# Optimization experiments

Measured on AMD Instinct MI355X. Metric: run time of the kernel, lower is better.

## Reference

```python
import jax, jax.numpy as jnp
import numpy as np

B, S, D, H, MLP = 8, 1024, 768, 12, 3072
HD = D // H
EPS = 1e-5


def setup_inputs() -> dict:
    key = jax.random.key(0)
    ks = jax.random.split(key, 5)
    sd = lambda fan_in: 1.0 / np.sqrt(fan_in)
    return {
        "x": jax.random.normal(ks[0], (B, S, D), jnp.float32),
        "w_qkv": jax.random.normal(ks[1], (D, 3 * D), jnp.float32) * sd(D),
        "w_out": jax.random.normal(ks[2], (D, D), jnp.float32) * sd(D),
        "b_out": jnp.zeros((D,), jnp.float32),
        "w1": jax.random.normal(ks[3], (D, MLP), jnp.float32) * sd(D),
        "b1": jnp.zeros((MLP,), jnp.float32),
        "w2": jax.random.normal(ks[4], (MLP, D), jnp.float32) * sd(MLP),
        "b2": jnp.zeros((D,), jnp.float32),
    }


def _instance_norm(x):
    # torch InstanceNorm2d on a 3D [B,S,D] tensor treats it as unbatched (C,H,W):
    # normalize over (S, D) per batch element, biased var, eps=1e-5, no affine.
    mu = jnp.mean(x, axis=(1, 2), keepdims=True)
    var = jnp.mean(jnp.square(x - mu), axis=(1, 2), keepdims=True)
    return (x - mu) * jax.lax.rsqrt(var + EPS)


def reference(x, w_qkv, w_out, b_out, w1, b1, w2, b2):
    scale = HD ** -0.5
    # --- self-attention branch ---
    h = _instance_norm(x)
    qkv = (h @ w_qkv).reshape(B, S, 3, H, HD)          # (qkv, heads, head_dim) split
    qkv = qkv.transpose(2, 0, 3, 1, 4)                  # [3, B, H, S, HD]
    q, k, v = qkv[0], qkv[1], qkv[2]
    att = jax.nn.softmax(jnp.einsum('bhxd,bhyd->bhxy', q, k) * scale, axis=-1)
    o = jnp.einsum('bhxy,bhyd->bhxd', att, v)           # [B, H, S, HD]
    o = o.transpose(0, 2, 1, 3).reshape(B, S, D)        # b h l d -> b l (h d)
    x = x + (o @ w_out + b_out)
    # --- MLP branch (exact erf GELU, as nn.GELU default) ---
    h2 = _instance_norm(x)
    m = jax.nn.gelu(h2 @ w1 + b1, approximate=False) @ w2 + b2
    return x + m
```

## Files before the change

kernel.cpp:

```cpp
#include <hip/hip_runtime.h>
#include <hip/hip_bf16.h>

typedef __hip_bfloat16 bf16;
typedef __attribute__((ext_vector_type(8))) short short8;
typedef __attribute__((ext_vector_type(4))) float f32x4;

#define B_   8
#define S_   1024
#define D_   768
#define H_   12
#define HD_  64
#define MLP_ 3072
#define SD_  (S_ * D_)

#define QSCALE 0.18033688011112042f

__device__ __forceinline__ float b2f(short h) {
  union { unsigned u; float f; } w;
  w.u = ((unsigned)(unsigned short)h) << 16;
  return w.f;
}

__device__ __forceinline__ void gl2lds16(const bf16* g, bf16* l) {
  __builtin_amdgcn_global_load_lds(
      (const __attribute__((address_space(1))) unsigned*)(const void*)g,
      (__attribute__((address_space(3))) unsigned*)(void*)l, 16, 0, 0);
}

__global__ __launch_bounds__(256) void transpose_all(
    const float* __restrict__ w_qkv, const float* __restrict__ w_out,
    const float* __restrict__ w1, const float* __restrict__ w2,
    bf16* __restrict__ t_qkv, bf16* __restrict__ t_out,
    bf16* __restrict__ t1, bf16* __restrict__ t2) {
  const int t = blockIdx.x;
  const float* in; bf16* out; int R, C, idx;
  if (t < 1728)      { in = w_qkv; out = t_qkv; R = 768;  C = 2304; idx = t; }
  else if (t < 2304) { in = w_out; out = t_out; R = 768;  C = 768;  idx = t - 1728; }
  else if (t < 4608) { in = w1;    out = t1;    R = 768;  C = 3072; idx = t - 2304; }
  else               { in = w2;    out = t2;    R = 3072; C = 768;  idx = t - 4608; }
  const int nbx = C >> 5;
  const int bx = (idx % nbx) * 32, by = (idx / nbx) * 32;
  __shared__ float tt[32][33];
  const int tx = threadIdx.x & 31, ty = threadIdx.x >> 5;
#pragma unroll
  for (int rr = 0; rr < 32; rr += 8)
    tt[ty + rr][tx] = in[(long)(by + ty + rr) * C + bx + tx];
  __syncthreads();
#pragma unroll
  for (int rr = 0; rr < 32; rr += 8)
    out[(long)(bx + ty + rr) * R + by + tx] = __float2bfloat16(tt[tx][ty + rr]);
}

__global__ __launch_bounds__(256) void stats_partial(const float* __restrict__ x,
                                                     float* __restrict__ redp,
                                                     const bf16* __restrict__ wt1,
                                                     float* __restrict__ cs1) {
  if (blockIdx.x >= 768) {
    const int bi = blockIdx.x - 768;
    const int row = bi * 64 + (threadIdx.x >> 2);
    const int part = threadIdx.x & 3;
    const bf16* wr = wt1 + (long)row * 768 + part * 192;
    float s = 0.f;
#pragma unroll
    for (int u = 0; u < 24; ++u) {
      short8 v = *(const short8*)(wr + u * 8);
#pragma unroll
      for (int e = 0; e < 8; ++e) s += b2f(v[e]);
    }
    s += __shfl_xor(s, 1, 64);
    s += __shfl_xor(s, 2, 64);
    if (part == 0) cs1[row] = s;
    return;
  }
  const long off = (long)blockIdx.x * 8192;
  float s = 0.f, s2 = 0.f;
#pragma unroll
  for (int it = 0; it < 8; ++it) {
    float4 v = *(const float4*)(x + off + ((long)threadIdx.x + it * 256) * 4);
    s += v.x + v.y + v.z + v.w;
    s2 += v.x * v.x + v.y * v.y + v.z * v.z + v.w * v.w;
  }
#pragma unroll
  for (int o = 1; o < 64; o <<= 1) { s += __shfl_xor(s, o, 64); s2 += __shfl_xor(s2, o, 64); }
  __shared__ float sh[8];
  const int wave = threadIdx.x >> 6, lane = threadIdx.x & 63;
  if (lane == 0) { sh[wave * 2] = s; sh[wave * 2 + 1] = s2; }
  __syncthreads();
  if (threadIdx.x == 0) {
    redp[blockIdx.x * 2]     = sh[0] + sh[2] + sh[4] + sh[6];
    redp[blockIdx.x * 2 + 1] = sh[1] + sh[3] + sh[5] + sh[7];
  }
}

__global__ __launch_bounds__(512) void stats_final(const float* __restrict__ redp,
                                                   float* __restrict__ red_x,
                                                   float* __restrict__ red2) {
  const int b = threadIdx.x >> 6, lane = threadIdx.x & 63;
  const int i0 = (b * 96 + lane) * 2;
  float s  = redp[i0]     + ((lane < 32) ? redp[i0 + 128]     : 0.f);
  float s2 = redp[i0 + 1] + ((lane < 32) ? redp[i0 + 128 + 1] : 0.f);
#pragma unroll
  for (int o = 1; o < 64; o <<= 1) { s += __shfl_xor(s, o, 64); s2 += __shfl_xor(s2, o, 64); }
  if (lane == 0) { red_x[b * 2] = s; red_x[b * 2 + 1] = s2; }
  if (threadIdx.x < 16) red2[threadIdx.x] = 0.f;
}

__global__ __launch_bounds__(256) void norm_k(const float* __restrict__ x,
                                              const float* __restrict__ sums,
                                              bf16* __restrict__ h) {
  const long i = ((long)blockIdx.x * 256 + threadIdx.x) * 8;
  const int b = (int)(i / SD_);
  const float mu = sums[b * 2] * (1.0f / SD_);
  const float var = sums[b * 2 + 1] * (1.0f / SD_) - mu * mu;
  const float rs = rsqrtf(var + 1e-5f);
  float4 v0 = *(const float4*)(x + i);
  float4 v1 = *(const float4*)(x + i + 4);
  __align__(16) bf16 tmp[8];
  tmp[0] = __float2bfloat16((v0.x - mu) * rs);
  tmp[1] = __float2bfloat16((v0.y - mu) * rs);
  tmp[2] = __float2bfloat16((v0.z - mu) * rs);
  tmp[3] = __float2bfloat16((v0.w - mu) * rs);
  tmp[4] = __float2bfloat16((v1.x - mu) * rs);
  tmp[5] = __float2bfloat16((v1.y - mu) * rs);
  tmp[6] = __float2bfloat16((v1.z - mu) * rs);
  tmp[7] = __float2bfloat16((v1.w - mu) * rs);
  *(short8*)(h + i) = *(const short8*)tmp;
}

template <int EPI, bool STATS>
__global__ __launch_bounds__(256) void gemm_k(
    const bf16* __restrict__ A, const bf16* __restrict__ Bt,
    int M, int N, int K,
    const float* __restrict__ biasf, const float* __restrict__ resf,
    const float* __restrict__ cs, const float* __restrict__ stat_in,
    float* __restrict__ outf,
    bf16* __restrict__ outb0, bf16* __restrict__ outb1, bf16* __restrict__ outb2,
    float* __restrict__ statp) {
  __shared__ __align__(16) bf16 As[2][128 * 64];
  __shared__ __align__(16) bf16 Bs[2][64 * 64];
  __shared__ float sred[8];
  const int tid = threadIdx.x;
  const int bm = blockIdx.x * 128, bn = blockIdx.y * 64;
  const int wave = tid >> 6, lane = tid & 63;
  const int quad = lane >> 4, l16 = lane & 15;
  const int wm = (wave >> 1) * 64, wn = (wave & 1) * 32;
  const int swz = l16 & 7;

  f32x4 acc[4][2];
#pragma unroll
  for (int i = 0; i < 4; ++i)
#pragma unroll
    for (int j = 0; j < 2; ++j) acc[i][j] = (f32x4){0.f, 0.f, 0.f, 0.f};

  const int srow = tid >> 3;
  const int sgc = (tid & 7) ^ (srow & 7);
  const bf16* Ab = A + (long)(bm + srow) * K + sgc * 8;
  const bf16* Bb = Bt + (long)(bn + srow) * K + sgc * 8;

  auto stage = [&](int buf, int k0) {
#pragma unroll
    for (int s = 0; s < 4; ++s)
      gl2lds16(Ab + (long)(s * 32) * K + k0, &As[buf][0] + s * 2048 + tid * 8);
#pragma unroll
    for (int s = 0; s < 2; ++s)
      gl2lds16(Bb + (long)(s * 32) * K + k0, &Bs[buf][0] + s * 2048 + tid * 8);
  };

  stage(0, 0);
  const int nk = K >> 6;
  for (int kt = 0; kt < nk; ++kt) {
    const int cur = kt & 1;
    __syncthreads();
    if (kt + 1 < nk) stage(cur ^ 1, (kt + 1) * 64);
    short8 a[2][4], b[2][2];
#pragma unroll
    for (int kk = 0; kk < 2; ++kk) {
      const int co = ((kk * 4 + quad) ^ swz) * 8;
#pragma unroll
      for (int i = 0; i < 4; ++i)
        a[kk][i] = *(const short8*)(&As[cur][0] + (wm + i * 16 + l16) * 64 + co);
#pragma unroll
      for (int j = 0; j < 2; ++j)
        b[kk][j] = *(const short8*)(&Bs[cur][0] + (wn + j * 16 + l16) * 64 + co);
    }
#pragma unroll
    for (int kk = 0; kk < 2; ++kk)
#pragma unroll
      for (int i = 0; i < 4; ++i)
#pragma unroll
        for (int j = 0; j < 2; ++j)
          acc[i][j] = __builtin_amdgcn_mfma_f32_16x16x32_bf16(a[kk][i], b[kk][j], acc[i][j], 0, 0, 0);
  }

  const int m0 = bm + wm + quad * 4;
  const int n0 = bn + wn + l16;
  const int batch = bm >> 10;
  float mu = 0.f, rs = 0.f;
  if (EPI == 2) {
    const float s1 = stat_in[batch * 2], s2v = stat_in[batch * 2 + 1];
    mu = s1 * (1.0f / SD_);
    rs = rsqrtf(s2v * (1.0f / SD_) - mu * mu + 1e-5f);
  }
  float ts = 0.f, ts2 = 0.f;
#pragma unroll
  for (int i = 0; i < 4; ++i) {
#pragma unroll
    for (int j = 0; j < 2; ++j) {
      const int n = n0 + j * 16;
#pragma unroll
      for (int r = 0; r < 4; ++r) {
        const int m = m0 + i * 16 + r;
        float v = acc[i][j][r];
        if (EPI == 0) {
          const int t = n / D_;
          const int rr2 = n - t * D_;
          const int hh = rr2 >> 6, dd = rr2 & 63;
          const int bb = m >> 10, ss = m & 1023;
          const long hoff = (long)(bb * H_ + hh);
          if (t == 0)      outb0[(hoff * S_ + ss) * HD_ + dd] = __float2bfloat16(v * QSCALE);
          else if (t == 1) outb1[(hoff * S_ + ss) * HD_ + dd] = __float2bfloat16(v);
          else             outb2[(hoff * HD_ + dd) * S_ + ss] = __float2bfloat16(v);
        } else if (EPI == 1) {
          v += biasf[n] + resf[(long)m * N + n];
          outf[(long)m * N + n] = v;
          outb0[(long)m * N + n] = __float2bfloat16(v);
          if (STATS) { ts += v; ts2 += v * v; }
        } else if (EPI == 2) {
          v = rs * (v - mu * cs[n]) + biasf[n];
          float u = v * v;
          float y = v * (1.0f + 0.044715f * u) * 0.7978845608028654f;
          float z = exp2f(y * -2.885390081777927f);
          v = v * __builtin_amdgcn_rcpf(1.0f + z);
          outb0[(long)m * N + n] = __float2bfloat16(v);
        } else {
          v += biasf[n] + resf[(long)m * N + n];
          outf[(long)m * N + n] = v;
        }
      }
    }
  }
  if (STATS) {
#pragma unroll
    for (int o = 1; o < 64; o <<= 1) { ts += __shfl_xor(ts, o, 64); ts2 += __shfl_xor(ts2, o, 64); }
    if (lane == 0) { sred[wave * 2] = ts; sred[wave * 2 + 1] = ts2; }
    __syncthreads();
    if (tid == 0) {
      atomicAdd(&statp[batch * 2], sred[0] + sred[2] + sred[4] + sred[6]);
      atomicAdd(&statp[batch * 2 + 1], sred[1] + sred[3] + sred[5] + sred[7]);
    }
  }
}

__global__ __launch_bounds__(256) void attn64(const bf16* __restrict__ q,
                                              const bf16* __restrict__ k,
                                              const bf16* __restrict__ vt,
                                              bf16* __restrict__ o) {
  __shared__ __align__(16) bf16 Ks[2][64 * 64];
  __shared__ __align__(16) bf16 Vs[2][64 * 64];
  __shared__ __align__(16) bf16 Ps[4 * 16 * 64];
  const int bh = blockIdx.x, qt = blockIdx.y;
  const int tid = threadIdx.x, wave = tid >> 6, lane = tid & 63;
  const int quad = lane >> 4, l16 = lane & 15;
  const int sw = (l16 & 7) ^ ((l16 >> 3) & 1);
  const long base = (long)bh * (S_ * HD_);
  const bf16* kg = k + base;
  const bf16* vg = vt + base;

  const int srow = tid >> 3;
  const int scg = (tid & 7) ^ (srow & 7) ^ ((srow >> 3) & 1);

  short8 aq[2];
#pragma unroll
  for (int kk = 0; kk < 2; ++kk)
    aq[kk] = *(const short8*)(q + base + (long)(qt * 64 + wave * 16 + l16) * HD_ +
                              kk * 32 + quad * 8);

  gl2lds16(kg + (long)srow * HD_ + scg * 8, &Ks[0][0] + tid * 8);
  gl2lds16(kg + (long)(32 + srow) * HD_ + scg * 8, &Ks[0][0] + 2048 + tid * 8);
  gl2lds16(vg + (long)srow * S_ + scg * 8, &Vs[0][0] + tid * 8);
  gl2lds16(vg + (long)(32 + srow) * S_ + scg * 8, &Vs[0][0] + 2048 + tid * 8);

  f32x4 oacc[4];
#pragma unroll
  for (int j = 0; j < 4; ++j) oacc[j] = (f32x4){0.f, 0.f, 0.f, 0.f};
  float lp = 0.f;

  for (int c = 0; c < 16; ++c) {
    const int cur = c & 1;
    __syncthreads();

    f32x4 s[4];
#pragma unroll
    for (int i = 0; i < 4; ++i) s[i] = (f32x4){0.f, 0.f, 0.f, 0.f};
#pragma unroll
    for (int kk = 0; kk < 2; ++kk) {
#pragma unroll
      for (int i = 0; i < 4; ++i) {
        short8 ak = *(const short8*)(&Ks[cur][0] + (i * 16 + l16) * 64 +
                                     (((kk * 4 + quad) ^ sw) * 8));
        s[i] = __builtin_amdgcn_mfma_f32_16x16x32_bf16(ak, aq[kk], s[i], 0, 0, 0);
      }
    }

    if (c < 15) {
      const int nxt = cur ^ 1;
      gl2lds16(kg + (long)((c + 1) * 64 + srow) * HD_ + scg * 8, &Ks[nxt][0] + tid * 8);
      gl2lds16(kg + (long)((c + 1) * 64 + 32 + srow) * HD_ + scg * 8, &Ks[nxt][0] + 2048 + tid * 8);
      gl2lds16(vg + (long)srow * S_ + (c + 1) * 64 + scg * 8, &Vs[nxt][0] + tid * 8);
      gl2lds16(vg + (long)(32 + srow) * S_ + (c + 1) * 64 + scg * 8, &Vs[nxt][0] + 2048 + tid * 8);
    }

#pragma unroll
    for (int i = 0; i < 4; ++i) {
      __align__(8) bf16 pk[4];
#pragma unroll
      for (int r = 0; r < 4; ++r) {
        float p = exp2f(s[i][r]);
        lp += p;
        pk[r] = __float2bfloat16(p);
      }
      const int chunk = 2 * i + (quad >> 1);
      *(uint2*)(Ps + wave * 1024 + l16 * 64 + ((chunk ^ sw) * 8) + (quad & 1) * 4) =
          *(const uint2*)pk;
    }

#pragma unroll
    for (int kk = 0; kk < 2; ++kk) {
      short8 ap = *(const short8*)(Ps + wave * 1024 + l16 * 64 +
                                   (((kk * 4 + quad) ^ sw) * 8));
#pragma unroll
      for (int dj = 0; dj < 4; ++dj) {
        short8 bv = *(const short8*)(&Vs[cur][0] + (dj * 16 + l16) * 64 +
                                     (((kk * 4 + quad) ^ sw) * 8));
        oacc[dj] = __builtin_amdgcn_mfma_f32_16x16x32_bf16(ap, bv, oacc[dj], 0, 0, 0);
      }
    }
  }

  float lt = lp;
  lt += __shfl_xor(lt, 16, 64);
  lt += __shfl_xor(lt, 32, 64);

  const int b = bh / H_, hh = bh - b * H_;
#pragma unroll
  for (int r = 0; r < 4; ++r) {
    const float inv = 1.0f / __shfl(lt, quad * 4 + r, 64);
    const int sg = qt * 64 + wave * 16 + quad * 4 + r;
    const long rowoff = ((long)b * S_ + sg) * D_ + hh * HD_;
#pragma unroll
    for (int dj = 0; dj < 4; ++dj)
      o[rowoff + dj * 16 + l16] = __float2bfloat16(oacc[dj][r] * inv);
  }
}

extern "C" void kernel_launch(void* const* d_in, const int* in_sizes, int n_in,
                              void* d_out, int out_size, void* d_ws, size_t ws_size,
                              hipStream_t stream) {
  const float* x     = (const float*)d_in[0];
  const float* w_qkv = (const float*)d_in[1];
  const float* w_out = (const float*)d_in[2];
  const float* b_out = (const float*)d_in[3];
  const float* w1    = (const float*)d_in[4];
  const float* b1    = (const float*)d_in[5];
  const float* w2    = (const float*)d_in[6];
  const float* b2    = (const float*)d_in[7];
  float* out = (float*)d_out;

  bf16* wt_qkv = (bf16*)d_ws;
  bf16* wt_out = wt_qkv + 2304 * 768;
  bf16* wt1    = wt_out + 768 * 768;
  bf16* wt2    = wt1 + 3072 * 768;
  bf16* qb     = wt2 + 768 * 3072;
  bf16* kb     = qb + 6291456;
  bf16* vtb    = kb + 6291456;
  bf16* ob     = vtb + 6291456;
  float* x1f   = (float*)(ob + 6291456);
  bf16* hb     = (bf16*)(x1f + 6291456);
  float* redp  = (float*)(hb + 6291456);
  float* red_x = redp + 1536;
  float* red2  = red_x + 16;
  float* cs1   = red2 + 16;
  bf16* gb     = qb;
  bf16* x1b    = hb;

  transpose_all<<<6912, 256, 0, stream>>>(w_qkv, w_out, w1, w2,
                                          wt_qkv, wt_out, wt1, wt2);

  stats_partial<<<768 + 48, 256, 0, stream>>>(x, redp, wt1, cs1);
  stats_final<<<1, 512, 0, stream>>>(redp, red_x, red2);
  norm_k<<<3072, 256, 0, stream>>>(x, red_x, hb);

  gemm_k<0, false><<<dim3(64, 36), 256, 0, stream>>>(
      hb, wt_qkv, 8192, 2304, 768, nullptr, nullptr, nullptr, nullptr,
      nullptr, qb, kb, vtb, nullptr);
  attn64<<<dim3(B_ * H_, 16), 256, 0, stream>>>(qb, kb, vtb, ob);

  gemm_k<1, true><<<dim3(64, 12), 256, 0, stream>>>(
      ob, wt_out, 8192, 768, 768, b_out, x, nullptr, nullptr,
      x1f, x1b, nullptr, nullptr, red2);

  gemm_k<2, false><<<dim3(64, 48), 256, 0, stream>>>(
      x1b, wt1, 8192, 3072, 768, b1, nullptr, cs1, red2,
      nullptr, gb, nullptr, nullptr, nullptr);

  gemm_k<3, false><<<dim3(64, 12), 256, 0, stream>>>(
      gb, wt2, 8192, 768, 3072, b2, x1f, nullptr, nullptr,
      out, nullptr, nullptr, nullptr, nullptr);
}
```

Baseline: 354.4 us.

## Load GEMM B-operand fragments directly to registers and raise occupancy hint

The B tile no longer goes through shared memory. Each wave now loads its B fragments straight from global memory into registers, with a register double-buffer prefetching the next k-step, and launch bounds now request 4 blocks per CU. This removes the LDS traffic and capacity used by B so more blocks can fit per CU. The trade-off is that waves sharing the same B columns now load them redundantly from global memory (two waves share each wn slice), uncoalesced 16-byte loads strided by K are issued per lane, and the extra registers may spill under the tighter launch bound.

Result: slower. 469.0 us (+32.3%).

```diff
diff --git a/kernel.cpp b/kernel.cpp
--- a/kernel.cpp
+++ b/kernel.cpp
@@ -128,7 +128,7 @@
 }
 
 template <int EPI, bool STATS>
-__global__ __launch_bounds__(256) void gemm_k(
+__global__ __launch_bounds__(256, 4) void gemm_k(
     const bf16* __restrict__ A, const bf16* __restrict__ Bt,
     int M, int N, int K,
     const float* __restrict__ biasf, const float* __restrict__ resf,
@@ -137,7 +137,6 @@
     bf16* __restrict__ outb0, bf16* __restrict__ outb1, bf16* __restrict__ outb2,
     float* __restrict__ statp) {
   __shared__ __align__(16) bf16 As[2][128 * 64];
-  __shared__ __align__(16) bf16 Bs[2][64 * 64];
   __shared__ float sred[8];
   const int tid = threadIdx.x;
   const int bm = blockIdx.x * 128, bn = blockIdx.y * 64;
@@ -155,41 +154,56 @@
   const int srow = tid >> 3;
   const int sgc = (tid & 7) ^ (srow & 7);
   const bf16* Ab = A + (long)(bm + srow) * K + sgc * 8;
-  const bf16* Bb = Bt + (long)(bn + srow) * K + sgc * 8;
-
-  auto stage = [&](int buf, int k0) {
+
+  auto stageA = [&](int buf, int k0) {
 #pragma unroll
     for (int s = 0; s < 4; ++s)
       gl2lds16(Ab + (long)(s * 32) * K + k0, &As[buf][0] + s * 2048 + tid * 8);
-#pragma unroll
-    for (int s = 0; s < 2; ++s)
-      gl2lds16(Bb + (long)(s * 32) * K + k0, &Bs[buf][0] + s * 2048 + tid * 8);
   };
 
-  stage(0, 0);
+  const bf16* Bg0 = Bt + (long)(bn + wn + l16) * K + quad * 8;
+  const bf16* Bg1 = Bg0 + (long)16 * K;
+
+  short8 bcur[2][2], bnxt[2][2];
+#pragma unroll
+  for (int kk = 0; kk < 2; ++kk) {
+    bcur[kk][0] = *(const short8*)(Bg0 + kk * 32);
+    bcur[kk][1] = *(const short8*)(Bg1 + kk * 32);
+  }
+  stageA(0, 0);
   const int nk = K >> 6;
   for (int kt = 0; kt < nk; ++kt) {
     const int cur = kt & 1;
     __syncthreads();
-    if (kt + 1 < nk) stage(cur ^ 1, (kt + 1) * 64);
-    short8 a[2][4], b[2][2];
+    if (kt + 1 < nk) {
+      stageA(cur ^ 1, (kt + 1) * 64);
+      const int k1 = (kt + 1) * 64;
+#pragma unroll
+      for (int kk = 0; kk < 2; ++kk) {
+        bnxt[kk][0] = *(const short8*)(Bg0 + k1 + kk * 32);
+        bnxt[kk][1] = *(const short8*)(Bg1 + k1 + kk * 32);
+      }
+    }
+    short8 a[2][4];
 #pragma unroll
     for (int kk = 0; kk < 2; ++kk) {
       const int co = ((kk * 4 + quad) ^ swz) * 8;
 #pragma unroll
       for (int i = 0; i < 4; ++i)
         a[kk][i] = *(const short8*)(&As[cur][0] + (wm + i * 16 + l16) * 64 + co);
+    }
+#pragma unroll
+    for (int kk = 0; kk < 2; ++kk)
+#pragma unroll
+      for (int i = 0; i < 4; ++i)
+#pragma unroll
+        for (int j = 0; j < 2; ++j)
+          acc[i][j] = __builtin_amdgcn_mfma_f32_16x16x32_bf16(a[kk][i], bcur[kk][j], acc[i][j], 0, 0, 0);
+#pragma unroll
+    for (int kk = 0; kk < 2; ++kk)
 #pragma unroll
       for (int j = 0; j < 2; ++j)
-        b[kk][j] = *(const short8*)(&Bs[cur][0] + (wn + j * 16 + l16) * 64 + co);
-    }
-#pragma unroll
-    for (int kk = 0; kk < 2; ++kk)
-#pragma unroll
-      for (int i = 0; i < 4; ++i)
-#pragma unroll
-        for (int j = 0; j < 2; ++j)
-          acc[i][j] = __builtin_amdgcn_mfma_f32_16x16x32_bf16(a[kk][i], b[kk][j], acc[i][j], 0, 0, 0);
+        bcur[kk][j] = bnxt[kk][j];
   }
 
   const int m0 = bm + wm + quad * 4;
```
